# Kernel optimization log

Measured on AMD Instinct MI355X. Metric: run time of the kernel, lower is better.

Reference implementation:

```python
import jax, jax.numpy as jnp
import numpy as np

ALPHA = 0.2  # LeakyReLU negative slope
NEG_INF = -1e9


def setup_inputs() -> dict:
    key = jax.random.key(0)
    k1, k2, k3, k4 = jax.random.split(key, 4)
    B, N, F_in, F_out = 4, 4096, 128, 128
    h = jax.random.normal(k1, (B, N, F_in), dtype=jnp.float32)
    adj = jax.random.randint(k2, (B, N, N), 0, 2, dtype=jnp.int32)
    # Xavier-uniform init matching nn.Linear weights
    limW = np.sqrt(6.0 / (F_in + F_out))
    W = jax.random.uniform(k3, (F_in, F_out), jnp.float32, -limW, limW)
    lima = np.sqrt(6.0 / (2 * F_out + 1))
    a = jax.random.uniform(k4, (2 * F_out,), jnp.float32, -lima, lima)
    return {"h": h, "adj": adj, "W": W, "a": a}


def reference(h, adj, W, a):
    # h: (B, N, F_in), adj: (B, N, N) int, W: (F_in, F_out), a: (2*F_out,)
    F_out = W.shape[1]
    Wh = jnp.einsum("bnf,fo->bno", h, W)  # (B, N, F_out)
    a_i, a_j = a[:F_out], a[F_out:]
    # e_ij = leakyrelu(a . [Wh_i, Wh_j]) = leakyrelu(a_i.Wh_i + a_j.Wh_j)
    si = Wh @ a_i  # (B, N) contribution of destination node i
    sj = Wh @ a_j  # (B, N) contribution of source node j
    e = si[:, :, None] + sj[:, None, :]  # (B, N, N)
    e = jnp.where(e > 0, e, ALPHA * e)  # LeakyReLU
    e = jnp.where(adj > 0, e, NEG_INF)  # masked scores
    attention = jax.nn.softmax(e, axis=-1)  # (B, N, N)
    # dropout is identity in eval mode
    h_prime = jnp.einsum("bij,bjo->bio", attention, Wh)  # (B, N, F_out)
    return jax.nn.elu(h_prime)  # concat=True -> ELU
```

## Files before the change

### kernel.cpp

```cpp
#include <hip/hip_runtime.h>

#define GN 4096
#define GF 128
#define GB 4

typedef __attribute__((ext_vector_type(8))) short short8;
typedef __attribute__((ext_vector_type(4))) float floatx4;

static __device__ __forceinline__ unsigned short f2bf(float x){
  unsigned int u = __float_as_uint(x);
  u += 0x7FFFu + ((u >> 16) & 1u);
  return (unsigned short)(u >> 16);
}

__global__ __launch_bounds__(256)
void gat_prep(const float* __restrict__ h, const float* __restrict__ W,
              const float* __restrict__ a, unsigned short* __restrict__ whB,
              float* __restrict__ si_g, unsigned short* __restrict__ EFh)
{
  __shared__ float hl[16*GF];
  __shared__ float red[2][2][16];
  const int tid = threadIdx.x;
  const int b   = blockIdx.x >> 8;
  const int r0  = (blockIdx.x & 255) << 4;
  const int o = tid & 127, g = tid >> 7;

  const float4* hb4 = (const float4*)(h + ((size_t)(b*GN + r0))*GF);
  ((float4*)hl)[tid]       = hb4[tid];
  ((float4*)hl)[tid + 256] = hb4[tid + 256];
  __syncthreads();

  float acc[8];
  #pragma unroll
  for (int r=0;r<8;++r) acc[r] = 0.f;
  const float* Wp = W + o;
  for (int f4=0; f4<32; ++f4){
    const float w0 = Wp[(f4*4+0)*GF];
    const float w1 = Wp[(f4*4+1)*GF];
    const float w2 = Wp[(f4*4+2)*GF];
    const float w3 = Wp[(f4*4+3)*GF];
    #pragma unroll
    for (int r=0;r<8;++r){
      const float4 h4 = *(const float4*)&hl[((g<<3)+r)*GF + (f4<<2)];
      acc[r] = fmaf(h4.x, w0, acc[r]);
      acc[r] = fmaf(h4.y, w1, acc[r]);
      acc[r] = fmaf(h4.z, w2, acc[r]);
      acc[r] = fmaf(h4.w, w3, acc[r]);
    }
  }

  const float ai = a[o], aj = a[GF + o];
  const int lane = tid & 63, wh = (tid >> 6) & 1;
  #pragma unroll
  for (int r=0;r<8;++r){
    float vi = acc[r]*ai, vj = acc[r]*aj;
    #pragma unroll
    for (int off=32; off; off>>=1){ vi += __shfl_down(vi, off); vj += __shfl_down(vj, off); }
    if (lane == 0){ red[0][wh][(g<<3)+r] = vi; red[1][wh][(g<<3)+r] = vj; }
  }

  unsigned short us[8] __attribute__((aligned(16)));
  #pragma unroll
  for (int r=0;r<8;++r) us[r] = f2bf(acc[r]);
  {
    const int j0 = r0 + (g<<3);
    unsigned short* dst = whB + (((size_t)(b*128 + (j0>>5))*128 + o)<<5) + (j0&31);
    *(uint4*)dst = *(const uint4*)us;
  }

  __syncthreads();
  if (tid < 16){
    si_g[b*GN + r0 + tid] = red[0][0][tid] + red[0][1][tid];
  } else if (tid < 32){
    const int r = tid - 16;
    const float vsj = red[1][0][r] + red[1][1][r];
    EFh[(size_t)b*8192 + r0 + r]        = f2bf(__expf(vsj));
    EFh[(size_t)b*8192 + 4096 + r0 + r] = f2bf(__expf(0.2f*vsj));
  }
}

__global__ __launch_bounds__(256, 3)
void gat_main(const int* __restrict__ adj, const unsigned short* __restrict__ whB,
              const float* __restrict__ si_g, const unsigned short* __restrict__ EFh,
              float* __restrict__ out)
{
  __shared__ __align__(16) char smem[16384 + 32*134*4];
  unsigned short* sEj = (unsigned short*)smem;
  unsigned int*   bitsW  = (unsigned int*)(smem + 16384);
  unsigned long long* bits64 = (unsigned long long*)(smem + 16384);
  float* smemc = (float*)smem;

  const int tid  = threadIdx.x;
  const int wave = tid >> 6, lane = tid & 63;
  const int b  = (blockIdx.x >> 1) & 3;
  const int i0 = ((((blockIdx.x >> 3) << 1) | (blockIdx.x & 1))) << 5;
  const int m = lane & 15, quad = lane >> 4, q8 = quad << 3;

  const int jw = wave << 10, jw32 = wave << 5;

  {
    const uint4* Eg = (const uint4*)(EFh + (size_t)b*8192);
    uint4* sE4 = (uint4*)sEj;
    #pragma unroll
    for (int k=0;k<4;++k) sE4[tid + (k<<8)] = Eg[tid + (k<<8)];
  }

  {
    const int* adjb = adj + ((size_t)(b*GN + i0))*GN + jw;
    #pragma unroll 2
    for (int r = 0; r < 32; ++r){
      const int* src = adjb + (size_t)r*GN;
      int v[16];
      #pragma unroll
      for (int c = 0; c < 16; ++c)
        v[c] = __builtin_nontemporal_load(src + (c<<6) + lane);
      #pragma unroll
      for (int c = 0; c < 16; ++c){
        const unsigned long long mm = __ballot(v[c] > 0);
        if (lane == 0) bits64[r*67 + (wave<<4) + c] = mm;
      }
    }
  }
  __syncthreads();

  const float si0 = si_g[(size_t)b*GN + i0 + m];
  const float si1 = si_g[(size_t)b*GN + i0 + 16 + m];
  const float Ti0 = __expf(-si0),      Ti1 = __expf(-si1);
  const float Ri0 = __expf(-0.8f*si0), Ri1 = __expf(-0.8f*si1);
  const unsigned short* lanebase = whB + ((size_t)b<<19) + (m<<5) + q8;

  floatx4 acc0[8], acc1[8];
  #pragma unroll
  for (int c=0;c<8;++c){ acc0[c] = (floatx4){0.f,0.f,0.f,0.f}; acc1[c] = (floatx4){0.f,0.f,0.f,0.f}; }
  floatx4 lf0 = (floatx4){0.f,0.f,0.f,0.f}, lf1 = (floatx4){0.f,0.f,0.f,0.f};
  const short8 ones8 = {0x3F80,0x3F80,0x3F80,0x3F80,0x3F80,0x3F80,0x3F80,0x3F80};

#define MKAF(dst_, sh_, Ti_, Ri_) do { \
    unsigned int aw[4]; \
    _Pragma("unroll") \
    for (int p=0;p<4;++p){ \
      unsigned int e0 = Eu[p] << 16, e1 = Eu[p] & 0xFFFF0000u; \
      unsigned int f0 = Fu[p] << 16, f1 = Fu[p] & 0xFFFF0000u; \
      float E0 = __uint_as_float(e0), E1 = __uint_as_float(e1); \
      float t0 = (Ri_)*__uint_as_float(f0), t1 = (Ri_)*__uint_as_float(f1); \
      float p0 = (E0 > (Ti_)) ? E0 : t0; \
      float p1 = (E1 > (Ti_)) ? E1 : t1; \
      unsigned int k0 = (unsigned int)(((int)((sh_) << (31-(2*p))))   >> 31); \
      unsigned int k1 = (unsigned int)(((int)((sh_) << (31-(2*p+1)))) >> 31); \
      unsigned int b0 = __float_as_uint(p0) & k0; \
      unsigned int b1 = __float_as_uint(p1) & k1; \
      aw[p] = ((b0 + 0x8000u) >> 16) | ((b1 + 0x8000u) & 0xFFFF0000u); \
    } \
    dst_ = *(const short8*)aw; \
  } while(0)

  #pragma unroll 2
  for (int it = 0; it < 32; ++it){
    const unsigned short* wb = lanebase + ((size_t)(jw32+it)<<12);
    short8 Bc[8];
    #pragma unroll
    for (int c=0;c<8;++c) Bc[c] = *(const short8*)(wb + (c<<9));

    const unsigned int sh0 = bitsW[m*134 + jw32 + it] >> q8;
    const unsigned int sh1 = bitsW[(m+16)*134 + jw32 + it] >> q8;
    const int jj = jw + (it << 5) + q8;
    const short8 Es = *(const short8*)&sEj[jj];
    const short8 Fs = *(const short8*)&sEj[4096 + jj];
    const unsigned int* Eu = (const unsigned int*)&Es;
    const unsigned int* Fu = (const unsigned int*)&Fs;
    short8 af0, af1;
    MKAF(af0, sh0, Ti0, Ri0);
    MKAF(af1, sh1, Ti1, Ri1);
    #pragma unroll
    for (int c=0;c<8;++c){
      acc0[c] = __builtin_amdgcn_mfma_f32_16x16x32_bf16(af0, Bc[c], acc0[c], 0, 0, 0);
      acc1[c] = __builtin_amdgcn_mfma_f32_16x16x32_bf16(af1, Bc[c], acc1[c], 0, 0, 0);
    }
    lf0 = __builtin_amdgcn_mfma_f32_16x16x32_bf16(af0, ones8, lf0, 0, 0, 0);
    lf1 = __builtin_amdgcn_mfma_f32_16x16x32_bf16(af1, ones8, lf1, 0, 0, 0);
  }
#undef MKAF

  #pragma unroll 1
  for (int g = 0; g < 2; ++g){
    __syncthreads();
    #pragma unroll
    for (int c=0;c<8;++c){
      #pragma unroll
      for (int r=0;r<4;++r){
        const float v = g ? acc1[c][r] : acc0[c][r];
        smemc[(wave*16 + quad*4 + r)*129 + c*16 + m] = v;
      }
    }
    if (m == 0){
      #pragma unroll
      for (int r=0;r<4;++r) smemc[8256 + wave*16 + quad*4 + r] = g ? lf1[r] : lf0[r];
    }
    __syncthreads();

    #pragma unroll
    for (int k=0;k<8;++k){
      const int idx = tid + (k<<8);
      const int row = idx >> 7, col = idx & 127;
      const float s = smemc[row*129+col] + smemc[(16+row)*129+col]
                    + smemc[(32+row)*129+col] + smemc[(48+row)*129+col];
      const float l = smemc[8256+row] + smemc[8256+16+row]
                    + smemc[8256+32+row] + smemc[8256+48+row];
      float v = s / l;
      v = v > 0.f ? v : expm1f(v);
      out[((size_t)(b*GN + i0 + (g<<4) + row))*GF + col] = v;
    }
  }
}

extern "C" void kernel_launch(void* const* d_in, const int* in_sizes, int n_in,
                              void* d_out, int out_size, void* d_ws, size_t ws_size,
                              hipStream_t stream)
{
  (void)in_sizes; (void)n_in; (void)out_size; (void)ws_size;
  const float* h   = (const float*)d_in[0];
  const int*   adj = (const int*)d_in[1];
  const float* W   = (const float*)d_in[2];
  const float* a   = (const float*)d_in[3];
  float* out = (float*)d_out;

  char* ws = (char*)d_ws;
  unsigned short* whB   = (unsigned short*)ws;
  float*          si    = (float*)(ws + (size_t)4*1024*1024);
  unsigned short* EFh   = (unsigned short*)(ws + (size_t)4*1024*1024 + 64*1024);

  gat_prep<<<GB*GN/16, 256, 0, stream>>>(h, W, a, whB, si, EFh);
  gat_main<<<GB*GN/32, 256, 0, stream>>>(adj, whB, si, EFh, out);
}
```

Before: 407.3 us.

## Pipeline adjacency loads and ballots with MFMA loop using double-buffered bitmasks

```diff
diff --git a/kernel.cpp b/kernel.cpp
--- a/kernel.cpp
+++ b/kernel.cpp
@@ -79,14 +79,13 @@
   }
 }
 
-__global__ __launch_bounds__(256, 3)
+__global__ __launch_bounds__(256, 2)
 void gat_main(const int* __restrict__ adj, const unsigned short* __restrict__ whB,
               const float* __restrict__ si_g, const unsigned short* __restrict__ EFh,
               float* __restrict__ out)
 {
-  __shared__ __align__(16) char smem[16384 + 32*134*4];
+  __shared__ __align__(16) char smem[34304];
   unsigned short* sEj = (unsigned short*)smem;
-  unsigned int*   bitsW  = (unsigned int*)(smem + 16384);
   unsigned long long* bits64 = (unsigned long long*)(smem + 16384);
   float* smemc = (float*)smem;
 
@@ -95,7 +94,6 @@
   const int b  = (blockIdx.x >> 1) & 3;
   const int i0 = ((((blockIdx.x >> 3) << 1) | (blockIdx.x & 1))) << 5;
   const int m = lane & 15, quad = lane >> 4, q8 = quad << 3;
-
   const int jw = wave << 10, jw32 = wave << 5;
 
   {
@@ -105,27 +103,14 @@
     for (int k=0;k<4;++k) sE4[tid + (k<<8)] = Eg[tid + (k<<8)];
   }
 
-  {
-    const int* adjb = adj + ((size_t)(b*GN + i0))*GN + jw;
-    #pragma unroll 2
-    for (int r = 0; r < 32; ++r){
-      const int* src = adjb + (size_t)r*GN;
-      int v[16];
-      #pragma unroll
-      for (int c = 0; c < 16; ++c)
-        v[c] = __builtin_nontemporal_load(src + (c<<6) + lane);
-      #pragma unroll
-      for (int c = 0; c < 16; ++c){
-        const unsigned long long mm = __ballot(v[c] > 0);
-        if (lane == 0) bits64[r*67 + (wave<<4) + c] = mm;
-      }
-    }
-  }
-  __syncthreads();
+  const int* adjb = adj + ((size_t)(b*GN + i0))*GN + jw + lane;
+
+  int vv[32];
+  #pragma unroll
+  for (int r=0;r<32;++r) vv[r] = __builtin_nontemporal_load(adjb + (size_t)r*GN);
 
   const float si0 = si_g[(size_t)b*GN + i0 + m];
   const float si1 = si_g[(size_t)b*GN + i0 + 16 + m];
-  const float Ti0 = __expf(-si0),      Ti1 = __expf(-si1);
   const float Ri0 = __expf(-0.8f*si0), Ri1 = __expf(-0.8f*si1);
   const unsigned short* lanebase = whB + ((size_t)b<<19) + (m<<5) + q8;
 
@@ -135,51 +120,88 @@
   floatx4 lf0 = (floatx4){0.f,0.f,0.f,0.f}, lf1 = (floatx4){0.f,0.f,0.f,0.f};
   const short8 ones8 = {0x3F80,0x3F80,0x3F80,0x3F80,0x3F80,0x3F80,0x3F80,0x3F80};
 
-#define MKAF(dst_, sh_, Ti_, Ri_) do { \
+#define BALLOTS(bufw_) do { \
+    unsigned long long* bw = bits64 + (((wave<<1) | (bufw_)) << 5); \
+    _Pragma("unroll") \
+    for (int r=0;r<32;++r){ \
+      const unsigned long long mm = __ballot(vv[r] > 0); \
+      if (lane == 0) bw[r] = mm; \
+    } \
+  } while(0)
+
+#define MKAF(dst_, sh_, Ri_) do { \
     unsigned int aw[4]; \
     _Pragma("unroll") \
     for (int p=0;p<4;++p){ \
-      unsigned int e0 = Eu[p] << 16, e1 = Eu[p] & 0xFFFF0000u; \
-      unsigned int f0 = Fu[p] << 16, f1 = Fu[p] & 0xFFFF0000u; \
-      float E0 = __uint_as_float(e0), E1 = __uint_as_float(e1); \
-      float t0 = (Ri_)*__uint_as_float(f0), t1 = (Ri_)*__uint_as_float(f1); \
-      float p0 = (E0 > (Ti_)) ? E0 : t0; \
-      float p1 = (E1 > (Ti_)) ? E1 : t1; \
-      unsigned int k0 = (unsigned int)(((int)((sh_) << (31-(2*p))))   >> 31); \
-      unsigned int k1 = (unsigned int)(((int)((sh_) << (31-(2*p+1)))) >> 31); \
-      unsigned int b0 = __float_as_uint(p0) & k0; \
-      unsigned int b1 = __float_as_uint(p1) & k1; \
+      const unsigned int e0 = Eu[p] << 16, e1 = Eu[p] & 0xFFFF0000u; \
+      const unsigned int f0 = Fu[p] << 16, f1 = Fu[p] & 0xFFFF0000u; \
+      const float p0 = fmaxf(__uint_as_float(e0), (Ri_)*__uint_as_float(f0)); \
+      const float p1 = fmaxf(__uint_as_float(e1), (Ri_)*__uint_as_float(f1)); \
+      const unsigned int k0 = (unsigned int)(((int)((sh_) << (31-(2*p))))   >> 31); \
+      const unsigned int k1 = (unsigned int)(((int)((sh_) << (31-(2*p+1)))) >> 31); \
+      const unsigned int b0 = __float_as_uint(p0) & k0; \
+      const unsigned int b1 = __float_as_uint(p1) & k1; \
       aw[p] = ((b0 + 0x8000u) >> 16) | ((b1 + 0x8000u) & 0xFFFF0000u); \
     } \
     dst_ = *(const short8*)aw; \
   } while(0)
 
-  #pragma unroll 2
-  for (int it = 0; it < 32; ++it){
-    const unsigned short* wb = lanebase + ((size_t)(jw32+it)<<12);
-    short8 Bc[8];
-    #pragma unroll
-    for (int c=0;c<8;++c) Bc[c] = *(const short8*)(wb + (c<<9));
-
-    const unsigned int sh0 = bitsW[m*134 + jw32 + it] >> q8;
-    const unsigned int sh1 = bitsW[(m+16)*134 + jw32 + it] >> q8;
-    const int jj = jw + (it << 5) + q8;
-    const short8 Es = *(const short8*)&sEj[jj];
-    const short8 Fs = *(const short8*)&sEj[4096 + jj];
-    const unsigned int* Eu = (const unsigned int*)&Es;
-    const unsigned int* Fu = (const unsigned int*)&Fs;
-    short8 af0, af1;
-    MKAF(af0, sh0, Ti0, Ri0);
-    MKAF(af1, sh1, Ti1, Ri1);
-    #pragma unroll
-    for (int c=0;c<8;++c){
-      acc0[c] = __builtin_amdgcn_mfma_f32_16x16x32_bf16(af0, Bc[c], acc0[c], 0, 0, 0);
-      acc1[c] = __builtin_amdgcn_mfma_f32_16x16x32_bf16(af1, Bc[c], acc1[c], 0, 0, 0);
-    }
-    lf0 = __builtin_amdgcn_mfma_f32_16x16x32_bf16(af0, ones8, lf0, 0, 0, 0);
-    lf1 = __builtin_amdgcn_mfma_f32_16x16x32_bf16(af1, ones8, lf1, 0, 0, 0);
-  }
+#define COMPUTE_T(cc_, t_, Bc_) do { \
+    const unsigned int* bwp = (const unsigned int*)(bits64 + (((wave<<1) | ((cc_)&1)) << 5)); \
+    const unsigned int sh0 = bwp[(m<<1) | (t_)] >> q8; \
+    const unsigned int sh1 = bwp[((m+16)<<1) | (t_)] >> q8; \
+    const int jj = jw + ((((cc_)<<1)|(t_))<<5) + q8; \
+    const short8 Es = *(const short8*)&sEj[jj]; \
+    const short8 Fs = *(const short8*)&sEj[4096 + jj]; \
+    const unsigned int* Eu = (const unsigned int*)&Es; \
+    const unsigned int* Fu = (const unsigned int*)&Fs; \
+    short8 af0, af1; \
+    MKAF(af0, sh0, Ri0); \
+    MKAF(af1, sh1, Ri1); \
+    _Pragma("unroll") \
+    for (int c=0;c<8;++c){ \
+      acc0[c] = __builtin_amdgcn_mfma_f32_16x16x32_bf16(af0, Bc_[c], acc0[c], 0, 0, 0); \
+      acc1[c] = __builtin_amdgcn_mfma_f32_16x16x32_bf16(af1, Bc_[c], acc1[c], 0, 0, 0); \
+    } \
+    lf0 = __builtin_amdgcn_mfma_f32_16x16x32_bf16(af0, ones8, lf0, 0, 0, 0); \
+    lf1 = __builtin_amdgcn_mfma_f32_16x16x32_bf16(af1, ones8, lf1, 0, 0, 0); \
+  } while(0)
+
+  __syncthreads();
+
+  BALLOTS(0);
+  asm volatile("s_waitcnt lgkmcnt(0)" ::: "memory");
+
+  #pragma unroll 1
+  for (int cc = 0; cc < 15; ++cc){
+    short8 Bc0[8], Bc1[8];
+    const unsigned short* wb0 = lanebase + ((size_t)(jw32 + (cc<<1)) << 12);
+    #pragma unroll
+    for (int c=0;c<8;++c) Bc0[c] = *(const short8*)(wb0 + (c<<9));
+    #pragma unroll
+    for (int c=0;c<8;++c) Bc1[c] = *(const short8*)(wb0 + 4096 + (c<<9));
+    #pragma unroll
+    for (int r=0;r<32;++r) vv[r] = __builtin_nontemporal_load(adjb + ((cc+1)<<6) + (size_t)r*GN);
+
+    COMPUTE_T(cc, 0, Bc0);
+    COMPUTE_T(cc, 1, Bc1);
+
+    BALLOTS((cc+1)&1);
+    asm volatile("s_waitcnt lgkmcnt(0)" ::: "memory");
+  }
+  {
+    short8 Bc0[8], Bc1[8];
+    const unsigned short* wb0 = lanebase + ((size_t)(jw32 + 30) << 12);
+    #pragma unroll
+    for (int c=0;c<8;++c) Bc0[c] = *(const short8*)(wb0 + (c<<9));
+    #pragma unroll
+    for (int c=0;c<8;++c) Bc1[c] = *(const short8*)(wb0 + 4096 + (c<<9));
+    COMPUTE_T(15, 0, Bc0);
+    COMPUTE_T(15, 1, Bc1);
+  }
+#undef COMPUTE_T
 #undef MKAF
+#undef BALLOTS
 
   #pragma unroll 1
   for (int g = 0; g < 2; ++g){
@@ -189,26 +211,34 @@
       #pragma unroll
       for (int r=0;r<4;++r){
         const float v = g ? acc1[c][r] : acc0[c][r];
-        smemc[(wave*16 + quad*4 + r)*129 + c*16 + m] = v;
+        smemc[(wave*16 + quad*4 + r)*132 + c*16 + m] = v;
       }
     }
     if (m == 0){
       #pragma unroll
-      for (int r=0;r<4;++r) smemc[8256 + wave*16 + quad*4 + r] = g ? lf1[r] : lf0[r];
+      for (int r=0;r<4;++r) smemc[8448 + wave*16 + quad*4 + r] = g ? lf1[r] : lf0[r];
     }
     __syncthreads();
 
-    #pragma unroll
-    for (int k=0;k<8;++k){
-      const int idx = tid + (k<<8);
-      const int row = idx >> 7, col = idx & 127;
-      const float s = smemc[row*129+col] + smemc[(16+row)*129+col]
-                    + smemc[(32+row)*129+col] + smemc[(48+row)*129+col];
-      const float l = smemc[8256+row] + smemc[8256+16+row]
-                    + smemc[8256+32+row] + smemc[8256+48+row];
-      float v = s / l;
-      v = v > 0.f ? v : expm1f(v);
-      out[((size_t)(b*GN + i0 + (g<<4) + row))*GF + col] = v;
+    const int rr = tid >> 5;
+    const int c4 = (tid & 31) << 2;
+    #pragma unroll
+    for (int hh = 0; hh < 2; ++hh){
+      const int row = rr + (hh<<3);
+      const float l = smemc[8448+row] + smemc[8448+16+row]
+                    + smemc[8448+32+row] + smemc[8448+48+row];
+      const float rl = __builtin_amdgcn_rcpf(l);
+      float4 o4;
+      #pragma unroll
+      for (int k=0;k<4;++k){
+        const int col = c4 + k;
+        const float s = smemc[row*132+col] + smemc[(16+row)*132+col]
+                      + smemc[(32+row)*132+col] + smemc[(48+row)*132+col];
+        float v = s * rl;
+        v = v > 0.f ? v : expm1f(v);
+        ((float*)&o4)[k] = v;
+      }
+      *(float4*)&out[((size_t)(b*GN + i0 + (g<<4) + row))*GF + c4] = o4;
     }
   }
 }
```

After: 410.0 us. No clear change (+0.7%).
